# Kernel tuning notes

Hardware: AMD Instinct MI355X
Metric: run time of the kernel (lower is better)

Reference implementation:

```python
import jax, jax.numpy as jnp
import numpy as np

N = 50000
E = 800000
HID = 128
FILT = 128
NG = 50
CUTOFF = 10.0
LOG2 = float(np.log(2.0))


def shifted_softplus(x):
    return jax.nn.softplus(x) - LOG2


def setup_inputs() -> dict:
    key = jax.random.key(0)
    ks = jax.random.split(key, 12)
    s_hid = 1.0 / np.sqrt(HID)
    s_ng = 1.0 / np.sqrt(NG)
    s_f = 1.0 / np.sqrt(FILT)
    return {
        "h": jax.random.normal(ks[0], (N, HID), jnp.float32),
        "pos": jax.random.normal(ks[1], (N, 3), jnp.float32),
        "edge_index": jax.random.randint(ks[2], (2, E), 0, N, jnp.int64),
        # edge filter MLP: Linear(NG->FILT), ssp, Linear(FILT->FILT)
        "mlp_w1": jax.random.uniform(ks[3], (NG, FILT), jnp.float32, -s_ng, s_ng),
        "mlp_b1": jax.random.uniform(ks[4], (FILT,), jnp.float32, -s_ng, s_ng),
        "mlp_w2": jax.random.uniform(ks[5], (FILT, FILT), jnp.float32, -s_f, s_f),
        "mlp_b2": jax.random.uniform(ks[6], (FILT,), jnp.float32, -s_f, s_f),
        # CFConv lin1 (no bias), lin2
        "lin1_w": jax.random.uniform(ks[7], (HID, FILT), jnp.float32, -s_hid, s_hid),
        "lin2_w": jax.random.uniform(ks[8], (FILT, HID), jnp.float32, -s_f, s_f),
        "lin2_b": jax.random.uniform(ks[9], (HID,), jnp.float32, -s_f, s_f),
        # InteractionBlock output linear
        "lin_w": jax.random.uniform(ks[10], (HID, HID), jnp.float32, -s_hid, s_hid),
        "lin_b": jax.random.uniform(ks[11], (HID,), jnp.float32, -s_hid, s_hid),
    }


def reference(h, pos, edge_index, mlp_w1, mlp_b1, mlp_w2, mlp_b2,
              lin1_w, lin2_w, lin2_b, lin_w, lin_b):
    row, col = edge_index[0], edge_index[1]  # target, source (PyG convention)

    # edge distances  [E]
    edge_weight = jnp.linalg.norm(pos[row] - pos[col], axis=-1)

    # GaussianSmearing: offsets linspace(0, cutoff, NG)  -> [E, NG]
    offset = jnp.linspace(0.0, CUTOFF, NG, dtype=h.dtype)
    coeff = -0.5 / (offset[1] - offset[0]) ** 2
    edge_attr = jnp.exp(coeff * (edge_weight[:, None] - offset) ** 2)

    # CFConv: cosine cutoff * filter MLP   -> edge filters W [E, FILT]
    C = 0.5 * (jnp.cos(edge_weight * (jnp.pi / CUTOFF)) + 1.0)
    W = shifted_softplus(edge_attr @ mlp_w1 + mlp_b1) @ mlp_w2 + mlp_b2
    W = W * C[:, None]

    # gather-modulate-scatter message passing
    x = h @ lin1_w                    # [N, FILT]
    msg = x[col] * W                  # [E, FILT]
    agg = jax.ops.segment_sum(msg, row, num_segments=N)  # [N, FILT]
    x = agg @ lin2_w + lin2_b         # [N, HID]

    # InteractionBlock tail
    x = shifted_softplus(x)
    x = x @ lin_w + lin_b
    return x
```

## Files before the change

kernel.cpp:

```cpp
#include <hip/hip_runtime.h>
#include <hip/hip_bf16.h>
#include <math.h>

#define HID   128
#define NG    50
#define TN    8192
#define TMAXD 16.0f
#define RPB   8
#define TSPB  16
#define TBLB  512
#define NRG   16
#define NSL   32
#define SCAN_CHUNK 1024

typedef __attribute__((ext_vector_type(8))) short bf16x8;
typedef __attribute__((ext_vector_type(4))) float f32x4;
typedef __attribute__((ext_vector_type(4))) int   i32x4;
typedef unsigned short u16;
typedef unsigned int   u32;

#define LOG2F 0.69314718056f

__device__ __forceinline__ float sspf(float v) {
    if (v > 15.f) return v - LOG2F;
    return __logf(1.f + __expf(v)) - LOG2F;
}

__device__ __forceinline__ u16 f2bf(float f) {
    __hip_bfloat16 h = __float2bfloat16(f);
    return *reinterpret_cast<u16*>(&h);
}
__device__ __forceinline__ float bf2f(u32 v) {
    union { u32 u; float f; } x; x.u = v << 16; return x.f;
}

union K1Smem {
    struct { float sattr[TSPB][64]; float st1[TSPB][128]; } tb;
    int hcnt[3328];
};

__global__ __launch_bounds__(256) void k1_table_hist_prep(
    const float* __restrict__ w1, const float* __restrict__ b1,
    const float* __restrict__ w2, const float* __restrict__ b2,
    u16* __restrict__ Tn,
    const int* __restrict__ eidx, int* __restrict__ cntp,
    const float* __restrict__ pos, u32* __restrict__ rec,
    const float* __restrict__ lin1, const float* __restrict__ lin2,
    const float* __restrict__ linw,
    u16* __restrict__ lin1T, u16* __restrict__ lin2T, u16* __restrict__ linwT,
    int N, int E)
{
    __shared__ K1Smem sm;

    const int tid = threadIdx.x;
    const int b   = blockIdx.x;

    if (b < TBLB) {
        const int s0 = b * TSPB;
        const float TSTEP = TMAXD / TN;
        const float GSTEP = 10.0f / 49.0f;
        const float COEFF = -0.5f / (GSTEP * GSTEP);

        for (int idx = tid; idx < TSPB * 64; idx += 256) {
            int s = idx >> 6, g = idx & 63;
            float v = 0.f;
            if (g < NG) {
                float d = (float)(s0 + s) * TSTEP;
                float t = d - (float)g * GSTEP;
                v = __expf(COEFF * t * t);
            }
            sm.tb.sattr[s][g] = v;
        }
        __syncthreads();

        const int c  = tid & 127;
        const int sh = tid >> 7;

        for (int s = sh; s < TSPB; s += 2) {
            float acc = b1[c];
#pragma unroll
            for (int g = 0; g < NG; ++g)
                acc = fmaf(sm.tb.sattr[s][g], w1[g * 128 + c], acc);
            sm.tb.st1[s][c] = sspf(acc);
        }
        __syncthreads();

        for (int s = sh; s < TSPB; s += 2) {
            float acc = b2[c];
#pragma unroll 8
            for (int k = 0; k < 128; ++k)
                acc = fmaf(sm.tb.st1[s][k], w2[k * 128 + c], acc);
            float d = (float)(s0 + s) * TSTEP;
            float Cf = 0.5f * (__cosf(d * 0.31415926535f) + 1.0f);
            Tn[(size_t)(s0 + s) * HID + c] = f2bf(acc * Cf);
        }
    } else if (b < TBLB + NRG * NSL) {
        int* hcnt = sm.hcnt;
        const int hb  = b - TBLB;
        const int rg  = hb / NSL;
        const int sl  = hb % NSL;
        const int rph = (N + NRG - 1) / NRG;
        const int lo  = rg * rph;
        const int hi  = min(lo + rph, N);
        const int nr  = hi - lo;

        for (int i = tid; i < nr; i += 256) hcnt[i] = 0;
        __syncthreads();

        const int esz = (E / NSL) & ~3;
        const int es  = sl * esz;
        const int ee  = (sl == NSL - 1) ? E : es + esz;
        const int n4  = (ee - es) >> 2;
        const i32x4* p4 = reinterpret_cast<const i32x4*>(eidx + es);
        for (int i = tid; i < n4; i += 256) {
            i32x4 v = p4[i];
#pragma unroll
            for (int j = 0; j < 4; ++j) {
                u32 rr = (u32)(v[j] - lo);
                if (rr < (u32)nr) atomicAdd(&hcnt[rr], 1);
            }
        }
        for (int e = es + (n4 << 2) + tid; e < ee; e += 256) {
            u32 rr = (u32)(eidx[e] - lo);
            if (rr < (u32)nr) atomicAdd(&hcnt[rr], 1);
        }
        __syncthreads();

        for (int i = tid; i < nr; i += 256)
            cntp[(size_t)sl * N + lo + i] = hcnt[i];
    } else if (b < TBLB + NRG * NSL + 192) {
        const int wt  = b - TBLB - NRG * NSL;
        const int wid = wt >> 6;
        const int t   = (wt & 63) * 256 + tid;
        const int n = t >> 7, k = t & 127;
        const float* src = (wid == 0) ? lin1 : (wid == 1) ? lin2 : linw;
        u16* dst = (wid == 0) ? lin1T : (wid == 1) ? lin2T : linwT;
        dst[t] = f2bf(src[k * 128 + n]);
    } else {
        const int rb = b - TBLB - NRG * NSL - 192;
        const int e  = rb * 256 + tid;
        if (e < E) {
            int r = eidx[e], c = eidx[E + e];
            float dx = pos[3 * r + 0] - pos[3 * c + 0];
            float dy = pos[3 * r + 1] - pos[3 * c + 1];
            float dz = pos[3 * r + 2] - pos[3 * c + 2];
            float d = sqrtf(dx * dx + dy * dy + dz * dz);
            int idx = (int)(d * (TN / TMAXD) + 0.5f);
            idx = min(idx, TN - 1);
            rec[e] = ((u32)idx << 16) | (u32)c;
        }
    }
}

__global__ __launch_bounds__(256) void k2_part_mfma(
    int* __restrict__ cntp, int* __restrict__ cnt, int* __restrict__ part,
    int nch,
    const float* __restrict__ h, const u16* __restrict__ lin1T,
    u16* __restrict__ bx, int N)
{
    __shared__ u16 sA[64 * 128];
    __shared__ int red[256];
    const int tid = threadIdx.x;

    if ((int)blockIdx.x < nch) {
        const int b = blockIdx.x;
        int base = b * SCAN_CHUNK + tid * 4;
        int s = 0;
#pragma unroll
        for (int i = 0; i < 4; ++i) {
            int idx = base + i;
            if (idx < N) {
                int run = 0;
#pragma unroll
                for (int sl = 0; sl < NSL; ++sl) {
                    int v = cntp[(size_t)sl * N + idx];
                    cntp[(size_t)sl * N + idx] = run;
                    run += v;
                }
                cnt[idx] = run;
                s += run;
            }
        }
        red[tid] = s;
        __syncthreads();
        for (int off = 128; off > 0; off >>= 1) {
            if (tid < off) red[tid] += red[tid + off];
            __syncthreads();
        }
        if (tid == 0) part[b] = red[0];
        return;
    }

    const int r0 = ((int)blockIdx.x - nch) * 64;

    for (int i = tid; i < 64 * 16; i += 256) {
        int row = i >> 4, ck = i & 15;
        i32x4 pk = (i32x4){0, 0, 0, 0};
        if (r0 + row < N) {
            const float* src = h + (size_t)(r0 + row) * HID + ck * 8;
            f32x4 a = *reinterpret_cast<const f32x4*>(src);
            f32x4 c = *reinterpret_cast<const f32x4*>(src + 4);
            pk[0] = (int)((u32)f2bf(a[0]) | ((u32)f2bf(a[1]) << 16));
            pk[1] = (int)((u32)f2bf(a[2]) | ((u32)f2bf(a[3]) << 16));
            pk[2] = (int)((u32)f2bf(c[0]) | ((u32)f2bf(c[1]) << 16));
            pk[3] = (int)((u32)f2bf(c[2]) | ((u32)f2bf(c[3]) << 16));
        }
        int byteoff = row * 256 + ((ck * 16) ^ ((row & 7) << 4));
        *reinterpret_cast<i32x4*>(reinterpret_cast<char*>(sA) + byteoff) = pk;
    }
    __syncthreads();

    const int lane = tid & 63;
    const int wv   = tid >> 6;
    const int l15  = lane & 15;
    const int l4   = lane >> 4;

    bf16x8 bw[2][4];
#pragma unroll
    for (int nt = 0; nt < 2; ++nt)
#pragma unroll
        for (int s = 0; s < 4; ++s) {
            int n = wv * 32 + nt * 16 + l15;
            bw[nt][s] = *reinterpret_cast<const bf16x8*>(lin1T + n * 128 + s * 32 + l4 * 8);
        }

    f32x4 acc[4][2];
#pragma unroll
    for (int mt = 0; mt < 4; ++mt) { acc[mt][0] = (f32x4){0,0,0,0}; acc[mt][1] = (f32x4){0,0,0,0}; }

#pragma unroll
    for (int mt = 0; mt < 4; ++mt)
#pragma unroll
        for (int s = 0; s < 4; ++s) {
            int e = mt * 16 + l15;
            int byteoff = e * 256 + ((s * 64 + l4 * 16) ^ ((e & 7) << 4));
            bf16x8 af = *reinterpret_cast<const bf16x8*>(reinterpret_cast<char*>(sA) + byteoff);
            acc[mt][0] = __builtin_amdgcn_mfma_f32_16x16x32_bf16(af, bw[0][s], acc[mt][0], 0, 0, 0);
            acc[mt][1] = __builtin_amdgcn_mfma_f32_16x16x32_bf16(af, bw[1][s], acc[mt][1], 0, 0, 0);
        }

#pragma unroll
    for (int mt = 0; mt < 4; ++mt)
#pragma unroll
        for (int nt = 0; nt < 2; ++nt)
#pragma unroll
            for (int r = 0; r < 4; ++r) {
                int row = r0 + mt * 16 + l4 * 4 + r;
                if (row < N)
                    bx[(size_t)row * HID + wv * 32 + nt * 16 + l15] = f2bf(acc[mt][nt][r]);
            }
}

__global__ __launch_bounds__(256) void scan_write(
    const int* __restrict__ cnt, const int* __restrict__ part,
    int* __restrict__ cur, int N)
{
    __shared__ int sc[256];
    int b = blockIdx.x, tid = threadIdx.x;
    int base = 0;
    for (int i = 0; i < b; ++i) base += part[i];
    int gbase = b * SCAN_CHUNK + tid * 4;
    int v[4];
#pragma unroll
    for (int i = 0; i < 4; ++i) { int idx = gbase + i; v[i] = (idx < N) ? cnt[idx] : 0; }
    int tsum = v[0] + v[1] + v[2] + v[3];
    sc[tid] = tsum;
    __syncthreads();
    for (int off = 1; off < 256; off <<= 1) {
        int add = (tid >= off) ? sc[tid - off] : 0;
        __syncthreads();
        sc[tid] += add;
        __syncthreads();
    }
    int tpre = base + sc[tid] - tsum;
    int run = 0;
#pragma unroll
    for (int i = 0; i < 4; ++i) {
        int idx = gbase + i;
        if (idx < N) cur[idx] = tpre + run;
        run += v[i];
    }
}

__global__ __launch_bounds__(256) void scatter_sorted(
    const int* __restrict__ eidx, const u32* __restrict__ rec,
    const int* __restrict__ cur, const int* __restrict__ cntp,
    u32* __restrict__ ec, int N, int E)
{
    __shared__ int lbase[3328];
    __shared__ int lcnt[3328];
    const int tid = threadIdx.x;
    const int rg  = blockIdx.x / NSL;
    const int sl  = blockIdx.x % NSL;
    const int rph = (N + NRG - 1) / NRG;
    const int lo  = rg * rph;
    const int hi  = min(lo + rph, N);
    const int nr  = hi - lo;

    for (int i = tid; i < nr; i += 256) {
        lbase[i] = cur[lo + i] + cntp[(size_t)sl * N + lo + i];
        lcnt[i]  = 0;
    }
    __syncthreads();

    const int esz = (E / NSL) & ~3;
    const int es  = sl * esz;
    const int ee  = (sl == NSL - 1) ? E : es + esz;
    const int n4  = (ee - es) >> 2;
    const i32x4* p4 = reinterpret_cast<const i32x4*>(eidx + es);
    for (int i = tid; i < n4; i += 256) {
        i32x4 v = p4[i];
#pragma unroll
        for (int j = 0; j < 4; ++j) {
            u32 rr = (u32)(v[j] - lo);
            if (rr < (u32)nr) {
                int o = atomicAdd(&lcnt[rr], 1);
                ec[lbase[rr] + o] = rec[es + (i << 2) + j];
            }
        }
    }
    for (int e = es + (n4 << 2) + tid; e < ee; e += 256) {
        u32 rr = (u32)(eidx[e] - lo);
        if (rr < (u32)nr) {
            int o = atomicAdd(&lcnt[rr], 1);
            ec[lbase[rr] + o] = rec[e];
        }
    }
}

__device__ __forceinline__ void eload4(
    const u32 v[4], const u16* __restrict__ Tn, const u16* __restrict__ bx,
    int c2, u32 T[4], u32 X[4])
{
#pragma unroll
    for (int j = 0; j < 4; ++j) {
        u32 rv = (u32)__builtin_amdgcn_readfirstlane((int)v[j]);
        int is = (int)(rv >> 16);
        int cs = (int)(rv & 0xffffu);
        T[j] = *reinterpret_cast<const u32*>(Tn + (size_t)is * HID + c2);
        X[j] = *reinterpret_cast<const u32*>(bx + (size_t)cs * HID + c2);
    }
}

__device__ __forceinline__ void efma4(
    const u32 T[4], const u32 X[4], float& ax, float& ay)
{
#pragma unroll
    for (int j = 0; j < 4; ++j) {
        ax = fmaf(bf2f(T[j] & 0xffffu), bf2f(X[j] & 0xffffu), ax);
        ay = fmaf(bf2f(T[j] >> 16), bf2f(X[j] >> 16), ay);
    }
}

__device__ __forceinline__ void eone(
    u32 v0, const u16* __restrict__ Tn, const u16* __restrict__ bx,
    int c2, float& ax, float& ay)
{
    u32 rv = (u32)__builtin_amdgcn_readfirstlane((int)v0);
    int is = (int)(rv >> 16);
    int cs = (int)(rv & 0xffffu);
    u32 T0 = *reinterpret_cast<const u32*>(Tn + (size_t)is * HID + c2);
    u32 X0 = *reinterpret_cast<const u32*>(bx + (size_t)cs * HID + c2);
    ax = fmaf(bf2f(T0 & 0xffffu), bf2f(X0 & 0xffffu), ax);
    ay = fmaf(bf2f(T0 >> 16), bf2f(X0 >> 16), ay);
}

__global__ __launch_bounds__(256) void edge_csr(
    const int* __restrict__ rowstart,
    const u32* __restrict__ ec,
    const u16* __restrict__ Tn,
    const u16* __restrict__ bx,
    float*     __restrict__ agg,
    int N, int E)
{
    const int lane = threadIdx.x & 63;
    const int slot = threadIdx.x >> 6;
    const int c2   = lane * 2;
    const int r0   = blockIdx.x * RPB;

    const int rA = r0 + slot;
    const int rB = r0 + 4 + slot;

    int eA = 0, eeA = 0, eB = 0, eeB = 0;
    if (rA < N) { eA = rowstart[rA]; eeA = (rA == N - 1) ? E : rowstart[rA + 1]; }
    if (rB < N) { eB = rowstart[rB]; eeB = (rB == N - 1) ? E : rowstart[rB + 1]; }

    float axA = 0.f, ayA = 0.f, axB = 0.f, ayB = 0.f;
    u32 vA[4], vB[4];
    u32 TA[4], TB[4];
    u32 XA[4], XB[4];

    while (eA + 4 <= eeA && eB + 4 <= eeB) {
#pragma unroll
        for (int j = 0; j < 4; ++j) { vA[j] = ec[eA + j]; vB[j] = ec[eB + j]; }
        eload4(vA, Tn, bx, c2, TA, XA);
        eload4(vB, Tn, bx, c2, TB, XB);
        efma4(TA, XA, axA, ayA);
        efma4(TB, XB, axB, ayB);
        eA += 4; eB += 4;
    }
    while (eA + 4 <= eeA) {
#pragma unroll
        for (int j = 0; j < 4; ++j) vA[j] = ec[eA + j];
        eload4(vA, Tn, bx, c2, TA, XA);
        efma4(TA, XA, axA, ayA);
        eA += 4;
    }
    for (; eA < eeA; ++eA) eone(ec[eA], Tn, bx, c2, axA, ayA);
    while (eB + 4 <= eeB) {
#pragma unroll
        for (int j = 0; j < 4; ++j) vB[j] = ec[eB + j];
        eload4(vB, Tn, bx, c2, TB, XB);
        efma4(TB, XB, axB, ayB);
        eB += 4;
    }
    for (; eB < eeB; ++eB) eone(ec[eB], Tn, bx, c2, axB, ayB);

    if (rA < N) {
        float2 o; o.x = axA; o.y = ayA;
        *reinterpret_cast<float2*>(agg + (size_t)rA * HID + c2) = o;
    }
    if (rB < N) {
        float2 o; o.x = axB; o.y = ayB;
        *reinterpret_cast<float2*>(agg + (size_t)rB * HID + c2) = o;
    }
}

__global__ __launch_bounds__(256) void tail_mfma(
    const float* __restrict__ agg,
    const u16* __restrict__ lin2T, const float* __restrict__ l2b,
    const u16* __restrict__ linwT, const float* __restrict__ linb,
    float* __restrict__ out, int N)
{
    __shared__ u16 sA[64 * 128];
    __shared__ u16 sT[64 * 128];

    const int tid = threadIdx.x;
    const int r0 = blockIdx.x * 64;

    for (int i = tid; i < 64 * 16; i += 256) {
        int row = i >> 4, ck = i & 15;
        i32x4 pk = (i32x4){0, 0, 0, 0};
        if (r0 + row < N) {
            const float* src = agg + (size_t)(r0 + row) * HID + ck * 8;
            f32x4 a = *reinterpret_cast<const f32x4*>(src);
            f32x4 c = *reinterpret_cast<const f32x4*>(src + 4);
            pk[0] = (int)((u32)f2bf(a[0]) | ((u32)f2bf(a[1]) << 16));
            pk[1] = (int)((u32)f2bf(a[2]) | ((u32)f2bf(a[3]) << 16));
            pk[2] = (int)((u32)f2bf(c[0]) | ((u32)f2bf(c[1]) << 16));
            pk[3] = (int)((u32)f2bf(c[2]) | ((u32)f2bf(c[3]) << 16));
        }
        int byteoff = row * 256 + ((ck * 16) ^ ((row & 7) << 4));
        *reinterpret_cast<i32x4*>(reinterpret_cast<char*>(sA) + byteoff) = pk;
    }
    __syncthreads();

    const int lane = tid & 63;
    const int wv   = tid >> 6;
    const int l15  = lane & 15;
    const int l4   = lane >> 4;
    const int n0   = wv * 32 + l15;
    const int n1   = n0 + 16;

    {
        bf16x8 bw[2][4];
#pragma unroll
        for (int nt = 0; nt < 2; ++nt)
#pragma unroll
            for (int s = 0; s < 4; ++s) {
                int n = wv * 32 + nt * 16 + l15;
                bw[nt][s] = *reinterpret_cast<const bf16x8*>(lin2T + n * 128 + s * 32 + l4 * 8);
            }

        f32x4 acc[4][2];
#pragma unroll
        for (int mt = 0; mt < 4; ++mt) { acc[mt][0] = (f32x4){0,0,0,0}; acc[mt][1] = (f32x4){0,0,0,0}; }

#pragma unroll
        for (int mt = 0; mt < 4; ++mt)
#pragma unroll
            for (int s = 0; s < 4; ++s) {
                int e = mt * 16 + l15;
                int byteoff = e * 256 + ((s * 64 + l4 * 16) ^ ((e & 7) << 4));
                bf16x8 af = *reinterpret_cast<const bf16x8*>(reinterpret_cast<char*>(sA) + byteoff);
                acc[mt][0] = __builtin_amdgcn_mfma_f32_16x16x32_bf16(af, bw[0][s], acc[mt][0], 0, 0, 0);
                acc[mt][1] = __builtin_amdgcn_mfma_f32_16x16x32_bf16(af, bw[1][s], acc[mt][1], 0, 0, 0);
            }

        const float bb0 = l2b[n0];
        const float bb1 = l2b[n1];
#pragma unroll
        for (int mt = 0; mt < 4; ++mt)
#pragma unroll
            for (int nt = 0; nt < 2; ++nt) {
                const int n = (nt == 0) ? n0 : n1;
                const float bb = (nt == 0) ? bb0 : bb1;
#pragma unroll
                for (int r = 0; r < 4; ++r) {
                    int m = mt * 16 + l4 * 4 + r;
                    float v = sspf(acc[mt][nt][r] + bb);
                    int byteoff = m * 256 + ((n * 2) ^ ((m & 7) << 4));
                    *reinterpret_cast<u16*>(reinterpret_cast<char*>(sT) + byteoff) = f2bf(v);
                }
            }
    }
    __syncthreads();

    {
        bf16x8 bw[2][4];
#pragma unroll
        for (int nt = 0; nt < 2; ++nt)
#pragma unroll
            for (int s = 0; s < 4; ++s) {
                int n = wv * 32 + nt * 16 + l15;
                bw[nt][s] = *reinterpret_cast<const bf16x8*>(linwT + n * 128 + s * 32 + l4 * 8);
            }

        f32x4 acc[4][2];
#pragma unroll
        for (int mt = 0; mt < 4; ++mt) { acc[mt][0] = (f32x4){0,0,0,0}; acc[mt][1] = (f32x4){0,0,0,0}; }

#pragma unroll
        for (int mt = 0; mt < 4; ++mt)
#pragma unroll
            for (int s = 0; s < 4; ++s) {
                int e = mt * 16 + l15;
                int byteoff = e * 256 + ((s * 64 + l4 * 16) ^ ((e & 7) << 4));
                bf16x8 af = *reinterpret_cast<const bf16x8*>(reinterpret_cast<char*>(sT) + byteoff);
                acc[mt][0] = __builtin_amdgcn_mfma_f32_16x16x32_bf16(af, bw[0][s], acc[mt][0], 0, 0, 0);
                acc[mt][1] = __builtin_amdgcn_mfma_f32_16x16x32_bf16(af, bw[1][s], acc[mt][1], 0, 0, 0);
            }

        const float cb0 = linb[n0];
        const float cb1 = linb[n1];
#pragma unroll
        for (int mt = 0; mt < 4; ++mt)
#pragma unroll
            for (int nt = 0; nt < 2; ++nt) {
                const int n = (nt == 0) ? n0 : n1;
                const float cb = (nt == 0) ? cb0 : cb1;
#pragma unroll
                for (int r = 0; r < 4; ++r) {
                    int row = r0 + mt * 16 + l4 * 4 + r;
                    if (row < N)
                        out[(size_t)row * HID + n] = acc[mt][nt][r] + cb;
                }
            }
    }
}

extern "C" void kernel_launch(void* const* d_in, const int* in_sizes, int n_in,
                              void* d_out, int out_size, void* d_ws, size_t ws_size,
                              hipStream_t stream)
{
    const float* h    = (const float*)d_in[0];
    const float* pos  = (const float*)d_in[1];
    const int*   eidx = (const int*)  d_in[2];
    const float* w1   = (const float*)d_in[3];
    const float* b1   = (const float*)d_in[4];
    const float* w2   = (const float*)d_in[5];
    const float* b2   = (const float*)d_in[6];
    const float* lin1 = (const float*)d_in[7];
    const float* lin2 = (const float*)d_in[8];
    const float* l2b  = (const float*)d_in[9];
    const float* linw = (const float*)d_in[10];
    const float* linb = (const float*)d_in[11];

    const int N = in_sizes[0] / HID;
    const int E = in_sizes[2] / 2;

    char* ws = (char*)d_ws;
    size_t off = 0;
    auto alloc = [&](size_t bytes) { char* p = ws + off; off = (off + bytes + 255) & ~(size_t)255; return p; };

    u16*    bx    = (u16*)   alloc((size_t)N * HID * sizeof(u16));
    u16*    Tn    = (u16*)   alloc((size_t)TN * HID * sizeof(u16));
    float*  agg   = (float*) alloc((size_t)N * HID * sizeof(float));
    int*    cntp  = (int*)   alloc((size_t)NSL * N * sizeof(int));
    int*    cnt   = (int*)   alloc((size_t)N * sizeof(int));
    int*    cur   = (int*)   alloc((size_t)N * sizeof(int));
    int*    part  = (int*)   alloc(256 * sizeof(int));
    u32*    rec   = (u32*)   alloc((size_t)E * sizeof(u32));
    u32*    ec    = (u32*)   alloc(((size_t)E + 8) * sizeof(u32));
    u16*    lin1T = (u16*)   alloc(128 * 128 * sizeof(u16));
    u16*    lin2T = (u16*)   alloc(128 * 128 * sizeof(u16));
    u16*    linwT = (u16*)   alloc(128 * 128 * sizeof(u16));

    const int nrec = (E + 255) / 256;

    k1_table_hist_prep<<<TBLB + NRG * NSL + 192 + nrec, 256, 0, stream>>>(
        w1, b1, w2, b2, Tn, eidx, cntp, pos, rec,
        lin1, lin2, linw, lin1T, lin2T, linwT, N, E);

    const int nch = (N + SCAN_CHUNK - 1) / SCAN_CHUNK;
    const int ngb = (N + 63) / 64;
    k2_part_mfma<<<nch + ngb, 256, 0, stream>>>(cntp, cnt, part, nch, h, lin1T, bx, N);

    scan_write<<<nch, 256, 0, stream>>>(cnt, part, cur, N);

    scatter_sorted<<<NRG * NSL, 256, 0, stream>>>(eidx, rec, cur, cntp, ec, N, E);

    edge_csr<<<(N + RPB - 1) / RPB, 256, 0, stream>>>(cur, ec, Tn, bx, agg, N, E);

    tail_mfma<<<ngb, 256, 0, stream>>>(agg, lin2T, l2b, linwT, linb, (float*)d_out, N);
}
```

Before: 150.6 us.

## Fuse CSR edge aggregation with MLP tail kernel via shared-memory tile

Merges the per-row edge gather/aggregate kernel with the two-layer tail MFMA kernel. Each block now aggregates 16 rows directly into a bf16 shared-memory tile and runs both 128x128 matmuls on it, so the fp32 agg buffer is never written to or read back from global memory and one launch goes away. In exchange, each block's MFMA tile shrinks from 64 rows to 16, so the lin2T and linwT weights are reloaded four times as often. The barrier-separated phases may also reduce overlap between the gather and the MFMA work.

```diff
diff --git a/kernel.cpp b/kernel.cpp
--- a/kernel.cpp
+++ b/kernel.cpp
@@ -6,7 +6,6 @@
 #define NG    50
 #define TN    8192
 #define TMAXD 16.0f
-#define RPB   8
 #define TSPB  16
 #define TBLB  512
 #define NRG   16
@@ -365,103 +364,79 @@
     ay = fmaf(bf2f(T0 >> 16), bf2f(X0 >> 16), ay);
 }
 
-__global__ __launch_bounds__(256) void edge_csr(
+__global__ __launch_bounds__(256) void edge_tail(
     const int* __restrict__ rowstart,
     const u32* __restrict__ ec,
     const u16* __restrict__ Tn,
     const u16* __restrict__ bx,
-    float*     __restrict__ agg,
-    int N, int E)
-{
-    const int lane = threadIdx.x & 63;
-    const int slot = threadIdx.x >> 6;
-    const int c2   = lane * 2;
-    const int r0   = blockIdx.x * RPB;
-
-    const int rA = r0 + slot;
-    const int rB = r0 + 4 + slot;
-
-    int eA = 0, eeA = 0, eB = 0, eeB = 0;
-    if (rA < N) { eA = rowstart[rA]; eeA = (rA == N - 1) ? E : rowstart[rA + 1]; }
-    if (rB < N) { eB = rowstart[rB]; eeB = (rB == N - 1) ? E : rowstart[rB + 1]; }
-
-    float axA = 0.f, ayA = 0.f, axB = 0.f, ayB = 0.f;
-    u32 vA[4], vB[4];
-    u32 TA[4], TB[4];
-    u32 XA[4], XB[4];
-
-    while (eA + 4 <= eeA && eB + 4 <= eeB) {
-#pragma unroll
-        for (int j = 0; j < 4; ++j) { vA[j] = ec[eA + j]; vB[j] = ec[eB + j]; }
-        eload4(vA, Tn, bx, c2, TA, XA);
-        eload4(vB, Tn, bx, c2, TB, XB);
-        efma4(TA, XA, axA, ayA);
-        efma4(TB, XB, axB, ayB);
-        eA += 4; eB += 4;
-    }
-    while (eA + 4 <= eeA) {
-#pragma unroll
-        for (int j = 0; j < 4; ++j) vA[j] = ec[eA + j];
-        eload4(vA, Tn, bx, c2, TA, XA);
-        efma4(TA, XA, axA, ayA);
-        eA += 4;
-    }
-    for (; eA < eeA; ++eA) eone(ec[eA], Tn, bx, c2, axA, ayA);
-    while (eB + 4 <= eeB) {
-#pragma unroll
-        for (int j = 0; j < 4; ++j) vB[j] = ec[eB + j];
-        eload4(vB, Tn, bx, c2, TB, XB);
-        efma4(TB, XB, axB, ayB);
-        eB += 4;
-    }
-    for (; eB < eeB; ++eB) eone(ec[eB], Tn, bx, c2, axB, ayB);
-
-    if (rA < N) {
-        float2 o; o.x = axA; o.y = ayA;
-        *reinterpret_cast<float2*>(agg + (size_t)rA * HID + c2) = o;
-    }
-    if (rB < N) {
-        float2 o; o.x = axB; o.y = ayB;
-        *reinterpret_cast<float2*>(agg + (size_t)rB * HID + c2) = o;
-    }
-}
-
-__global__ __launch_bounds__(256) void tail_mfma(
-    const float* __restrict__ agg,
     const u16* __restrict__ lin2T, const float* __restrict__ l2b,
     const u16* __restrict__ linwT, const float* __restrict__ linb,
-    float* __restrict__ out, int N)
-{
-    __shared__ u16 sA[64 * 128];
-    __shared__ u16 sT[64 * 128];
-
-    const int tid = threadIdx.x;
-    const int r0 = blockIdx.x * 64;
-
-    for (int i = tid; i < 64 * 16; i += 256) {
-        int row = i >> 4, ck = i & 15;
-        i32x4 pk = (i32x4){0, 0, 0, 0};
-        if (r0 + row < N) {
-            const float* src = agg + (size_t)(r0 + row) * HID + ck * 8;
-            f32x4 a = *reinterpret_cast<const f32x4*>(src);
-            f32x4 c = *reinterpret_cast<const f32x4*>(src + 4);
-            pk[0] = (int)((u32)f2bf(a[0]) | ((u32)f2bf(a[1]) << 16));
-            pk[1] = (int)((u32)f2bf(a[2]) | ((u32)f2bf(a[3]) << 16));
-            pk[2] = (int)((u32)f2bf(c[0]) | ((u32)f2bf(c[1]) << 16));
-            pk[3] = (int)((u32)f2bf(c[2]) | ((u32)f2bf(c[3]) << 16));
-        }
-        int byteoff = row * 256 + ((ck * 16) ^ ((row & 7) << 4));
-        *reinterpret_cast<i32x4*>(reinterpret_cast<char*>(sA) + byteoff) = pk;
+    float*     __restrict__ out,
+    int N, int E)
+{
+    __shared__ u16 sA[16 * 128];
+
+    const int lane = threadIdx.x & 63;
+    const int wv   = threadIdx.x >> 6;
+    const int c2   = lane * 2;
+    const int r0   = blockIdx.x * 16;
+
+#pragma unroll
+    for (int pp = 0; pp < 2; ++pp) {
+        const int mA = wv * 4 + pp * 2;
+        const int mB = mA + 1;
+        const int rA = r0 + mA;
+        const int rB = r0 + mB;
+
+        int eA = 0, eeA = 0, eB = 0, eeB = 0;
+        if (rA < N) { eA = rowstart[rA]; eeA = (rA == N - 1) ? E : rowstart[rA + 1]; }
+        if (rB < N) { eB = rowstart[rB]; eeB = (rB == N - 1) ? E : rowstart[rB + 1]; }
+
+        float axA = 0.f, ayA = 0.f, axB = 0.f, ayB = 0.f;
+        u32 vA[4], vB[4], TA[4], TB[4], XA[4], XB[4];
+
+        while (eA + 4 <= eeA && eB + 4 <= eeB) {
+#pragma unroll
+            for (int j = 0; j < 4; ++j) { vA[j] = ec[eA + j]; vB[j] = ec[eB + j]; }
+            eload4(vA, Tn, bx, c2, TA, XA);
+            eload4(vB, Tn, bx, c2, TB, XB);
+            efma4(TA, XA, axA, ayA);
+            efma4(TB, XB, axB, ayB);
+            eA += 4; eB += 4;
+        }
+        while (eA + 4 <= eeA) {
+#pragma unroll
+            for (int j = 0; j < 4; ++j) vA[j] = ec[eA + j];
+            eload4(vA, Tn, bx, c2, TA, XA);
+            efma4(TA, XA, axA, ayA);
+            eA += 4;
+        }
+        for (; eA < eeA; ++eA) eone(ec[eA], Tn, bx, c2, axA, ayA);
+        while (eB + 4 <= eeB) {
+#pragma unroll
+            for (int j = 0; j < 4; ++j) vB[j] = ec[eB + j];
+            eload4(vB, Tn, bx, c2, TB, XB);
+            efma4(TB, XB, axB, ayB);
+            eB += 4;
+        }
+        for (; eB < eeB; ++eB) eone(ec[eB], Tn, bx, c2, axB, ayB);
+
+        u32 pA = (u32)f2bf(axA) | ((u32)f2bf(ayA) << 16);
+        u32 pB = (u32)f2bf(axB) | ((u32)f2bf(ayB) << 16);
+        int boA = mA * 256 + ((c2 * 2) ^ ((mA & 7) << 4));
+        int boB = mB * 256 + ((c2 * 2) ^ ((mB & 7) << 4));
+        *reinterpret_cast<u32*>(reinterpret_cast<char*>(sA) + boA) = pA;
+        *reinterpret_cast<u32*>(reinterpret_cast<char*>(sA) + boB) = pB;
     }
     __syncthreads();
 
-    const int lane = tid & 63;
-    const int wv   = tid >> 6;
-    const int l15  = lane & 15;
-    const int l4   = lane >> 4;
-    const int n0   = wv * 32 + l15;
-    const int n1   = n0 + 16;
-
+    const int l15 = lane & 15;
+    const int l4  = lane >> 4;
+    const int n0  = wv * 32 + l15;
+    const int n1  = n0 + 16;
+
+    f32x4 acc0 = (f32x4){0, 0, 0, 0};
+    f32x4 acc1 = (f32x4){0, 0, 0, 0};
     {
         bf16x8 bw[2][4];
 #pragma unroll
@@ -471,41 +446,35 @@
                 int n = wv * 32 + nt * 16 + l15;
                 bw[nt][s] = *reinterpret_cast<const bf16x8*>(lin2T + n * 128 + s * 32 + l4 * 8);
             }
-
-        f32x4 acc[4][2];
-#pragma unroll
-        for (int mt = 0; mt < 4; ++mt) { acc[mt][0] = (f32x4){0,0,0,0}; acc[mt][1] = (f32x4){0,0,0,0}; }
-
-#pragma unroll
-        for (int mt = 0; mt < 4; ++mt)
-#pragma unroll
-            for (int s = 0; s < 4; ++s) {
-                int e = mt * 16 + l15;
-                int byteoff = e * 256 + ((s * 64 + l4 * 16) ^ ((e & 7) << 4));
-                bf16x8 af = *reinterpret_cast<const bf16x8*>(reinterpret_cast<char*>(sA) + byteoff);
-                acc[mt][0] = __builtin_amdgcn_mfma_f32_16x16x32_bf16(af, bw[0][s], acc[mt][0], 0, 0, 0);
-                acc[mt][1] = __builtin_amdgcn_mfma_f32_16x16x32_bf16(af, bw[1][s], acc[mt][1], 0, 0, 0);
-            }
-
+#pragma unroll
+        for (int s = 0; s < 4; ++s) {
+            int e = l15;
+            int byteoff = e * 256 + ((s * 64 + l4 * 16) ^ ((e & 7) << 4));
+            bf16x8 af = *reinterpret_cast<const bf16x8*>(reinterpret_cast<char*>(sA) + byteoff);
+            acc0 = __builtin_amdgcn_mfma_f32_16x16x32_bf16(af, bw[0][s], acc0, 0, 0, 0);
+            acc1 = __builtin_amdgcn_mfma_f32_16x16x32_bf16(af, bw[1][s], acc1, 0, 0, 0);
+        }
+    }
+    __syncthreads();
+
+    {
         const float bb0 = l2b[n0];
         const float bb1 = l2b[n1];
 #pragma unroll
-        for (int mt = 0; mt < 4; ++mt)
-#pragma unroll
-            for (int nt = 0; nt < 2; ++nt) {
-                const int n = (nt == 0) ? n0 : n1;
-                const float bb = (nt == 0) ? bb0 : bb1;
-#pragma unroll
-                for (int r = 0; r < 4; ++r) {
-                    int m = mt * 16 + l4 * 4 + r;
-                    float v = sspf(acc[mt][nt][r] + bb);
-                    int byteoff = m * 256 + ((n * 2) ^ ((m & 7) << 4));
-                    *reinterpret_cast<u16*>(reinterpret_cast<char*>(sT) + byteoff) = f2bf(v);
-                }
-            }
+        for (int r = 0; r < 4; ++r) {
+            int m = l4 * 4 + r;
+            float v0 = sspf(acc0[r] + bb0);
+            float v1 = sspf(acc1[r] + bb1);
+            int bo0 = m * 256 + ((n0 * 2) ^ ((m & 7) << 4));
+            int bo1 = m * 256 + ((n1 * 2) ^ ((m & 7) << 4));
+            *reinterpret_cast<u16*>(reinterpret_cast<char*>(sA) + bo0) = f2bf(v0);
+            *reinterpret_cast<u16*>(reinterpret_cast<char*>(sA) + bo1) = f2bf(v1);
+        }
     }
     __syncthreads();
 
+    acc0 = (f32x4){0, 0, 0, 0};
+    acc1 = (f32x4){0, 0, 0, 0};
     {
         bf16x8 bw[2][4];
 #pragma unroll
@@ -515,37 +484,26 @@
                 int n = wv * 32 + nt * 16 + l15;
                 bw[nt][s] = *reinterpret_cast<const bf16x8*>(linwT + n * 128 + s * 32 + l4 * 8);
             }
-
-        f32x4 acc[4][2];
-#pragma unroll
-        for (int mt = 0; mt < 4; ++mt) { acc[mt][0] = (f32x4){0,0,0,0}; acc[mt][1] = (f32x4){0,0,0,0}; }
-
-#pragma unroll
-        for (int mt = 0; mt < 4; ++mt)
-#pragma unroll
-            for (int s = 0; s < 4; ++s) {
-                int e = mt * 16 + l15;
-                int byteoff = e * 256 + ((s * 64 + l4 * 16) ^ ((e & 7) << 4));
-                bf16x8 af = *reinterpret_cast<const bf16x8*>(reinterpret_cast<char*>(sT) + byteoff);
-                acc[mt][0] = __builtin_amdgcn_mfma_f32_16x16x32_bf16(af, bw[0][s], acc[mt][0], 0, 0, 0);
-                acc[mt][1] = __builtin_amdgcn_mfma_f32_16x16x32_bf16(af, bw[1][s], acc[mt][1], 0, 0, 0);
-            }
-
+#pragma unroll
+        for (int s = 0; s < 4; ++s) {
+            int e = l15;
+            int byteoff = e * 256 + ((s * 64 + l4 * 16) ^ ((e & 7) << 4));
+            bf16x8 af = *reinterpret_cast<const bf16x8*>(reinterpret_cast<char*>(sA) + byteoff);
+            acc0 = __builtin_amdgcn_mfma_f32_16x16x32_bf16(af, bw[0][s], acc0, 0, 0, 0);
+            acc1 = __builtin_amdgcn_mfma_f32_16x16x32_bf16(af, bw[1][s], acc1, 0, 0, 0);
+        }
+    }
+    {
         const float cb0 = linb[n0];
         const float cb1 = linb[n1];
 #pragma unroll
-        for (int mt = 0; mt < 4; ++mt)
-#pragma unroll
-            for (int nt = 0; nt < 2; ++nt) {
-                const int n = (nt == 0) ? n0 : n1;
-                const float cb = (nt == 0) ? cb0 : cb1;
-#pragma unroll
-                for (int r = 0; r < 4; ++r) {
-                    int row = r0 + mt * 16 + l4 * 4 + r;
-                    if (row < N)
-                        out[(size_t)row * HID + n] = acc[mt][nt][r] + cb;
-                }
-            }
+        for (int r = 0; r < 4; ++r) {
+            int row = r0 + l4 * 4 + r;
+            if (row < N) {
+                out[(size_t)row * HID + n0] = acc0[r] + cb0;
+                out[(size_t)row * HID + n1] = acc1[r] + cb1;
+            }
+        }
     }
 }
 
@@ -575,7 +533,6 @@
 
     u16*    bx    = (u16*)   alloc((size_t)N * HID * sizeof(u16));
     u16*    Tn    = (u16*)   alloc((size_t)TN * HID * sizeof(u16));
-    float*  agg   = (float*) alloc((size_t)N * HID * sizeof(float));
     int*    cntp  = (int*)   alloc((size_t)NSL * N * sizeof(int));
     int*    cnt   = (int*)   alloc((size_t)N * sizeof(int));
     int*    cur   = (int*)   alloc((size_t)N * sizeof(int));
@@ -600,7 +557,8 @@
 
     scatter_sorted<<<NRG * NSL, 256, 0, stream>>>(eidx, rec, cur, cntp, ec, N, E);
 
-    edge_csr<<<(N + RPB - 1) / RPB, 256, 0, stream>>>(cur, ec, Tn, bx, agg, N, E);
-
-    tail_mfma<<<ngb, 256, 0, stream>>>(agg, lin2T, l2b, linwT, linb, (float*)d_out, N);
-}
+    const int ntile = (N + 15) / 16;
+    edge_tail<<<ntile, 256, 0, stream>>>(cur, ec, Tn, bx,
+                                         lin2T, l2b, linwT, linb,
+                                         (float*)d_out, N, E);
+}
```

Result: slower. 155.5 us (+3.2%).
